# Kernel optimization log

Measured on AMD Instinct MI355X. Metric: run time of the kernel, lower is better.

The kernel has to match this reference:

```python
import jax, jax.numpy as jnp
import numpy as np

T, B, OBS, A, P, NB, H = 32, 256, 1024, 16, 600, 601, 128


def setup_inputs() -> dict:
    key = jax.random.key(0)
    ks = jax.random.split(key, 32)
    f32 = jnp.float32

    def rn(k, shape, scale):
        return jax.random.normal(k, shape, dtype=f32) * scale

    hh = 1.0 / np.sqrt(H)
    inp = {
        "obs_seq": rn(ks[0], (T, B, OBS), 1.0),
        # backbone MLP (512, 512)
        "bb_w1": rn(ks[1], (OBS, 512), 1.0 / np.sqrt(OBS)), "bb_b1": jnp.zeros((512,), f32),
        "bb_w2": rn(ks[2], (512, 512), 1.0 / np.sqrt(512)), "bb_b2": jnp.zeros((512,), f32),
        # feedforward heads (final layers init std=0.01, bias 0 per module)
        "pol_w": rn(ks[3], (512, A), 0.01), "pol_b": jnp.zeros((A,), f32),
        "y_w": rn(ks[4], (512, P), 0.01), "y_b": jnp.zeros((P,), f32),
        "ci_w": rn(ks[5], (512, H), 1.0 / np.sqrt(512)), "ci_b": jnp.zeros((H,), f32),
        # LSTMCell(A, 128): gate order i,f,g,o as in torch
        "w_ih": rn(ks[6], (A, 4 * H), hh), "w_hh": rn(ks[7], (H, 4 * H), hh),
        "b_ih": rn(ks[8], (4 * H,), hh), "b_hh": rn(ks[9], (4 * H,), hh),
        # z / q / aux_pi MLPs: Linear(128,128) -> ReLU -> Linear(128, out)
        "z_w1": rn(ks[10], (H, H), hh), "z_b1": jnp.zeros((H,), f32),
        "z_w2": rn(ks[11], (H, P), 0.01), "z_b2": jnp.zeros((P,), f32),
        "q_w1": rn(ks[12], (H, H), hh), "q_b1": jnp.zeros((H,), f32),
        "q_w2": rn(ks[13], (H, NB), 0.01), "q_b2": jnp.zeros((NB,), f32),
        "a_w1": rn(ks[14], (H, H), hh), "a_b1": jnp.zeros((H,), f32),
        "a_w2": rn(ks[15], (H, A), 0.01), "a_b2": jnp.zeros((A,), f32),
    }
    return inp


def reference(obs_seq, bb_w1, bb_b1, bb_w2, bb_b2, pol_w, pol_b, y_w, y_b,
              ci_w, ci_b, w_ih, w_hh, b_ih, b_hh,
              z_w1, z_b1, z_w2, z_b2, q_w1, q_b1, q_w2, q_b2,
              a_w1, a_b1, a_w2, a_b2):
    Tn, Bn = obs_seq.shape[:2]
    x = obs_seq.reshape(Tn * Bn, -1)  # feedforward across time: fold T into batch
    emb = jax.nn.relu(jax.nn.relu(x @ bb_w1 + bb_b1) @ bb_w2 + bb_b2)  # [N,512]
    logits = emb @ pol_w + pol_b  # [N,A]
    y = emb @ y_w + y_b           # [N,P]
    c0 = emb @ ci_w + ci_b        # [N,H]
    h0 = jnp.tanh(c0)

    # one_hot(a) @ W_ih^T == row a of W_ih (input-to-gate contribution per action)
    in_gates = w_ih + b_ih  # [A, 4H]

    def step(carry, ig):
        h, c = carry
        g = ig + h @ w_hh + b_hh  # [N,4H]
        i, f, gg, o = jnp.split(g, 4, axis=-1)  # torch gate order i,f,g,o
        c = jax.nn.sigmoid(f) * c + jax.nn.sigmoid(i) * jnp.tanh(gg)
        h = jax.nn.sigmoid(o) * jnp.tanh(c)
        return (h, c), h

    _, h_all = jax.lax.scan(step, (h0, c0), in_gates)  # [A, N, H]

    def mlp(hx, w1, b1, w2, b2):
        return jax.nn.relu(hx @ w1 + b1) @ w2 + b2

    def to_tba(arr):
        Aa, N, D = arr.shape
        return arr.reshape(Aa, Tn, Bn, D).transpose(1, 2, 0, 3)  # [T,B,A,D]

    z = to_tba(mlp(h_all, z_w1, z_b1, z_w2, z_b2))
    q = to_tba(mlp(h_all, q_w1, q_b1, q_w2, q_b2))
    aux_pi = to_tba(mlp(h_all, a_w1, a_b1, a_w2, a_b2))
    return (logits.reshape(Tn, Bn, -1), y.reshape(Tn, Bn, -1), z, q, aux_pi)
```

## Files before the change

### kernel.cpp

```cpp
#include <hip/hip_runtime.h>
#include <stdint.h>

typedef short bf16x8 __attribute__((ext_vector_type(8)));
typedef float f32x4 __attribute__((ext_vector_type(4)));
typedef unsigned short u16x4 __attribute__((ext_vector_type(4)));

__device__ __forceinline__ unsigned short f2b(float f) {
  union { float f; unsigned u; } v; v.f = f;
  unsigned r = v.u + 0x7fffu + ((v.u >> 16) & 1u);
  return (unsigned short)(r >> 16);
}
__device__ __forceinline__ float fsigm(float x) { return 1.f / (1.f + __expf(-x)); }
__device__ __forceinline__ float ftanh(float x) {
  float t = __expf(-2.f * fabsf(x));
  float r = (1.f - t) / (1.f + t);
  return copysignf(r, x);
}

struct TD { const float* in; unsigned short* out; int R, C; };
struct TDs { TD d[12]; };

__global__ __launch_bounds__(256) void tconv_all(TDs ds) {
  TD t = ds.d[blockIdx.z];
  int c0 = blockIdx.x * 32, r0 = blockIdx.y * 32;
  if (c0 >= t.C || r0 >= t.R) return;
  __shared__ float tl[32][33];
  int tx = threadIdx.x & 31, ty = threadIdx.x >> 5;
  #pragma unroll
  for (int i = 0; i < 32; i += 8) {
    int r = r0 + ty + i, c = c0 + tx;
    tl[ty + i][tx] = (r < t.R && c < t.C) ? t.in[(size_t)r * t.C + c] : 0.f;
  }
  __syncthreads();
  #pragma unroll
  for (int i = 0; i < 32; i += 8) {
    int c = c0 + ty + i, r = r0 + tx;
    if (c < t.C && r < t.R) t.out[(size_t)c * t.R + r] = f2b(tl[tx][ty + i]);
  }
}

__global__ __launch_bounds__(256) void conv_k(const float* __restrict__ in,
                                              unsigned short* __restrict__ out, int n) {
  int i = (blockIdx.x * 256 + threadIdx.x) * 8;
  if (i >= n) return;
  float4 a = *(const float4*)(in + i);
  float4 b = *(const float4*)(in + i + 4);
  bf16x8 v;
  v[0] = (short)f2b(a.x); v[1] = (short)f2b(a.y); v[2] = (short)f2b(a.z); v[3] = (short)f2b(a.w);
  v[4] = (short)f2b(b.x); v[5] = (short)f2b(b.y); v[6] = (short)f2b(b.z); v[7] = (short)f2b(b.w);
  *(bf16x8*)(out + i) = v;
}

template <int ACT, bool OBF16>
__global__ __launch_bounds__(256) void gemm_k(const unsigned short* __restrict__ A,
                                              const unsigned short* __restrict__ BT,
                                              const float* __restrict__ bias,
                                              void* __restrict__ Cp,
                                              int M, int N, int K, int ldC) {
  __shared__ unsigned short As[64][40];
  __shared__ unsigned short Bs[64][40];
  const int tid = threadIdx.x;
  const int n0 = blockIdx.x * 64;
  const int m0 = blockIdx.y * 64;
  const int wid = tid >> 6, lane = tid & 63;
  const int wm = (wid >> 1) * 32, wn = (wid & 1) * 32;
  const int lr = lane & 15, lk = lane >> 4;
  const int sr = tid >> 2, sc = (tid & 3) * 8;

  f32x4 acc[2][2] = {};

  for (int k0 = 0; k0 < K; k0 += 32) {
    *(bf16x8*)&As[sr][sc] = *(const bf16x8*)(A + (size_t)(m0 + sr) * K + k0 + sc);
    {
      int n = n0 + sr;
      bf16x8 v = {};
      if (n < N) v = *(const bf16x8*)(BT + (size_t)n * K + k0 + sc);
      *(bf16x8*)&Bs[sr][sc] = v;
    }
    __syncthreads();
    bf16x8 af[2], bfr[2];
    #pragma unroll
    for (int mi = 0; mi < 2; mi++) af[mi] = *(const bf16x8*)&As[wm + mi * 16 + lr][lk * 8];
    #pragma unroll
    for (int ni = 0; ni < 2; ni++) bfr[ni] = *(const bf16x8*)&Bs[wn + ni * 16 + lr][lk * 8];
    #pragma unroll
    for (int mi = 0; mi < 2; mi++)
      #pragma unroll
      for (int ni = 0; ni < 2; ni++)
        acc[mi][ni] = __builtin_amdgcn_mfma_f32_16x16x32_bf16(af[mi], bfr[ni], acc[mi][ni], 0, 0, 0);
    __syncthreads();
  }

  #pragma unroll
  for (int mi = 0; mi < 2; mi++)
    #pragma unroll
    for (int ni = 0; ni < 2; ni++) {
      int col = n0 + wn + ni * 16 + lr;
      if (col >= N) continue;
      float bv = bias[col];
      #pragma unroll
      for (int r = 0; r < 4; r++) {
        int row = m0 + wm + mi * 16 + lk * 4 + r;
        float v = acc[mi][ni][r] + bv;
        if (ACT == 1) v = fmaxf(v, 0.f);
        if (OBF16) ((unsigned short*)Cp)[(size_t)row * ldC + col] = f2b(v);
        else       ((float*)Cp)[(size_t)row * ldC + col] = v;
      }
    }
}

__global__ __launch_bounds__(1024) void lstm_k(const float* __restrict__ c0,
                                               const unsigned short* __restrict__ whhT,
                                               const float* __restrict__ w_ih,
                                               const float* __restrict__ b_ih,
                                               const float* __restrict__ b_hh,
                                               unsigned short* __restrict__ h_all) {
  __shared__ float G[32][516];
  __shared__ float cst[32][128];
  __shared__ unsigned short hst[32][136];
  const int tid = threadIdx.x, lane = tid & 63, wid = tid >> 6;
  const int r0 = blockIdx.x * 32;
  const int lr = lane & 15, lk = lane >> 4;

  bf16x8 wv[2][4];
  #pragma unroll
  for (int nj = 0; nj < 2; nj++)
    #pragma unroll
    for (int ks = 0; ks < 4; ks++)
      wv[nj][ks] = *(const bf16x8*)(whhT + (size_t)(wid * 32 + nj * 16 + lr) * 128 + ks * 32 + lk * 8);

  const int j = tid & 127;
  const int rb = tid >> 7;
  const float bs0 = b_ih[j]       + b_hh[j];
  const float bs1 = b_ih[j + 128] + b_hh[j + 128];
  const float bs2 = b_ih[j + 256] + b_hh[j + 256];
  const float bs3 = b_ih[j + 384] + b_hh[j + 384];

  {
    int r = tid >> 5, j4 = (tid & 31) * 4;
    float4 c4 = *(const float4*)(c0 + (size_t)(r0 + r) * 128 + j4);
    *(f32x4*)&cst[r][j4] = f32x4{c4.x, c4.y, c4.z, c4.w};
    u16x4 h4;
    h4[0] = f2b(ftanh(c4.x)); h4[1] = f2b(ftanh(c4.y));
    h4[2] = f2b(ftanh(c4.z)); h4[3] = f2b(ftanh(c4.w));
    *(u16x4*)&hst[r][j4] = h4;
  }
  __syncthreads();

  for (int a = 0; a < 16; a++) {
    f32x4 acc[2][2] = {};
    #pragma unroll
    for (int ks = 0; ks < 4; ks++) {
      bf16x8 af0 = *(const bf16x8*)&hst[lr][ks * 32 + lk * 8];
      bf16x8 af1 = *(const bf16x8*)&hst[16 + lr][ks * 32 + lk * 8];
      #pragma unroll
      for (int nj = 0; nj < 2; nj++) {
        acc[0][nj] = __builtin_amdgcn_mfma_f32_16x16x32_bf16(af0, wv[nj][ks], acc[0][nj], 0, 0, 0);
        acc[1][nj] = __builtin_amdgcn_mfma_f32_16x16x32_bf16(af1, wv[nj][ks], acc[1][nj], 0, 0, 0);
      }
    }
    #pragma unroll
    for (int mi = 0; mi < 2; mi++)
      #pragma unroll
      for (int nj = 0; nj < 2; nj++)
        #pragma unroll
        for (int rr = 0; rr < 4; rr++)
          G[mi * 16 + lk * 4 + rr][wid * 32 + nj * 16 + lr] = acc[mi][nj][rr];
    __syncthreads();

    const float* ig = w_ih + a * 512;
    const float ig0 = ig[j], ig1 = ig[j + 128], ig2 = ig[j + 256], ig3 = ig[j + 384];
    #pragma unroll
    for (int it = 0; it < 4; it++) {
      int r = rb + it * 8;
      float gi = G[r][j]       + ig0 + bs0;
      float gf = G[r][j + 128] + ig1 + bs1;
      float gg = G[r][j + 256] + ig2 + bs2;
      float go = G[r][j + 384] + ig3 + bs3;
      float c = cst[r][j];
      float cn = fsigm(gf) * c + fsigm(gi) * ftanh(gg);
      float h = fsigm(go) * ftanh(cn);
      cst[r][j] = cn;
      unsigned short hb = f2b(h);
      hst[r][j] = hb;
      h_all[((size_t)(r0 + r) * 16 + a) * 128 + j] = hb;
    }
    __syncthreads();
  }
}

__global__ __launch_bounds__(64, 4) void heads_k(
    const unsigned short* __restrict__ hall,
    const unsigned short* __restrict__ w1cat,
    const unsigned short* __restrict__ w2cat,
    const float* __restrict__ zb1, const float* __restrict__ qb1, const float* __restrict__ ab1,
    const float* __restrict__ zb2, const float* __restrict__ qb2, const float* __restrict__ ab2,
    float* __restrict__ oz, float* __restrict__ oq, float* __restrict__ oa) {
  __shared__ unsigned short hp[32][136];
  const int lane = threadIdx.x & 63;
  const int lr = lane & 15, lk = lane >> 4;
  const int r0 = blockIdx.x * 32;

  const float* B1a[3] = {zb1, qb1, ab1};
  const float* B2a[3] = {zb2, qb2, ab2};
  float*       OOa[3] = {oz, oq, oa};

  #pragma unroll
  for (int hi = 0; hi < 3; hi++) {
    const int Nh    = (hi == 0) ? 600 : (hi == 1) ? 601 : 16;
    const int so    = (hi == 0) ? 0 : (hi == 1) ? 600 : 1201;
    const int NFULL = Nh >> 4;
    const int TAIL  = Nh & 15;
    const float* b1 = B1a[hi];
    const float* b2 = B2a[hi];
    float* Oh = OOa[hi];

    {
      bf16x8 av[2][4];
      #pragma unroll
      for (int jf = 0; jf < 2; jf++)
        #pragma unroll
        for (int ks = 0; ks < 4; ks++)
          av[jf][ks] = *(const bf16x8*)(hall + (size_t)(r0 + jf * 16 + lr) * 128 + ks * 32 + lk * 8);
      #pragma unroll
      for (int nf = 0; nf < 8; nf++) {
        bf16x8 w1v[4];
        #pragma unroll
        for (int ks = 0; ks < 4; ks++)
          w1v[ks] = *(const bf16x8*)(w1cat + (size_t)(hi * 128 + nf * 16 + lr) * 128 + ks * 32 + lk * 8);
        f32x4 hacc[2] = {};
        #pragma unroll
        for (int ks = 0; ks < 4; ks++)
          #pragma unroll
          for (int jf = 0; jf < 2; jf++)
            hacc[jf] = __builtin_amdgcn_mfma_f32_16x16x32_bf16(w1v[ks], av[jf][ks], hacc[jf], 0, 0, 0);
        f32x4 bb = *(const f32x4*)(b1 + nf * 16 + lk * 4);
        #pragma unroll
        for (int jf = 0; jf < 2; jf++) {
          u16x4 h4;
          #pragma unroll
          for (int rr = 0; rr < 4; rr++)
            h4[rr] = f2b(fmaxf(hacc[jf][rr] + bb[rr], 0.f));
          *(u16x4*)&hp[jf * 16 + lr][nf * 16 + lk * 4] = h4;
        }
      }
    }
    asm volatile("s_waitcnt lgkmcnt(0)" ::: "memory");
    __builtin_amdgcn_sched_barrier(0);

    bf16x8 hv[2][4];
    #pragma unroll
    for (int jf = 0; jf < 2; jf++)
      #pragma unroll
      for (int ks = 0; ks < 4; ks++)
        hv[jf][ks] = *(const bf16x8*)&hp[jf * 16 + lr][ks * 32 + lk * 8];

    bf16x8 wA[4], wB[4];
    {
      int rowb = min(lr, Nh - 1);
      #pragma unroll
      for (int ks = 0; ks < 4; ks++)
        wA[ks] = *(const bf16x8*)(w2cat + (size_t)(so + rowb) * 128 + ks * 32 + lk * 8);
    }
    const int NFT = NFULL + (TAIL ? 1 : 0);
    for (int fo = 0; fo < NFULL; fo++) {
      int fn = fo + 1;
      if (fn < NFT) {
        int rowb = min(fn * 16 + lr, Nh - 1);
        #pragma unroll
        for (int ks = 0; ks < 4; ks++)
          wB[ks] = *(const bf16x8*)(w2cat + (size_t)(so + rowb) * 128 + ks * 32 + lk * 8);
      }
      f32x4 oacc[2] = {};
      #pragma unroll
      for (int ks = 0; ks < 4; ks++)
        #pragma unroll
        for (int jf = 0; jf < 2; jf++)
          oacc[jf] = __builtin_amdgcn_mfma_f32_16x16x32_bf16(wA[ks], hv[jf][ks], oacc[jf], 0, 0, 0);
      f32x4 bb = *(const f32x4*)(b2 + fo * 16 + lk * 4);
      #pragma unroll
      for (int jf = 0; jf < 2; jf++) {
        f32x4 v = oacc[jf] + bb;
        float* p = Oh + (size_t)(r0 + jf * 16 + lr) * Nh + fo * 16 + lk * 4;
        __builtin_memcpy(p, &v, 16);
      }
      #pragma unroll
      for (int ks = 0; ks < 4; ks++) wA[ks] = wB[ks];
    }
    if (TAIL) {
      f32x4 oacc[2] = {};
      #pragma unroll
      for (int ks = 0; ks < 4; ks++)
        #pragma unroll
        for (int jf = 0; jf < 2; jf++)
          oacc[jf] = __builtin_amdgcn_mfma_f32_16x16x32_bf16(wA[ks], hv[jf][ks], oacc[jf], 0, 0, 0);
      #pragma unroll
      for (int jf = 0; jf < 2; jf++)
        #pragma unroll
        for (int rr = 0; rr < 4; rr++) {
          int col = NFULL * 16 + lk * 4 + rr;
          if (col < Nh)
            Oh[(size_t)(r0 + jf * 16 + lr) * Nh + col] = oacc[jf][rr] + b2[col];
        }
    }
  }
}

extern "C" void kernel_launch(void* const* d_in, const int* in_sizes, int n_in,
                              void* d_out, int out_size, void* d_ws, size_t ws_size,
                              hipStream_t stream) {
  const float* obs   = (const float*)d_in[0];
  const float* bb_w1 = (const float*)d_in[1];
  const float* bb_b1 = (const float*)d_in[2];
  const float* bb_w2 = (const float*)d_in[3];
  const float* bb_b2 = (const float*)d_in[4];
  const float* pol_w = (const float*)d_in[5];
  const float* pol_b = (const float*)d_in[6];
  const float* y_w   = (const float*)d_in[7];
  const float* y_b   = (const float*)d_in[8];
  const float* ci_w  = (const float*)d_in[9];
  const float* ci_b  = (const float*)d_in[10];
  const float* w_ih  = (const float*)d_in[11];
  const float* w_hh  = (const float*)d_in[12];
  const float* b_ih  = (const float*)d_in[13];
  const float* b_hh  = (const float*)d_in[14];
  const float* z_w1  = (const float*)d_in[15];
  const float* z_b1  = (const float*)d_in[16];
  const float* z_w2  = (const float*)d_in[17];
  const float* z_b2  = (const float*)d_in[18];
  const float* q_w1  = (const float*)d_in[19];
  const float* q_b1  = (const float*)d_in[20];
  const float* q_w2  = (const float*)d_in[21];
  const float* q_b2  = (const float*)d_in[22];
  const float* a_w1  = (const float*)d_in[23];
  const float* a_b1  = (const float*)d_in[24];
  const float* a_w2  = (const float*)d_in[25];
  const float* a_b2  = (const float*)d_in[26];

  float* out = (float*)d_out;
  float* out_logits = out;
  float* out_y      = out + 131072;
  float* out_z      = out + 5046272;
  float* out_q      = out + 83689472;
  float* out_a      = out + 162463744;

  uint8_t* ws = (uint8_t*)d_ws;
  size_t off = 0;
  auto alc = [&](size_t bytes) -> void* {
    void* p = ws + off;
    off = (off + bytes + 255) & ~(size_t)255;
    return p;
  };
  unsigned short* W1T  = (unsigned short*)alc((size_t)512 * 1024 * 2);
  unsigned short* W2T  = (unsigned short*)alc((size_t)512 * 512 * 2);
  unsigned short* polT = (unsigned short*)alc((size_t)16 * 512 * 2);
  unsigned short* yT   = (unsigned short*)alc((size_t)600 * 512 * 2);
  unsigned short* ciT  = (unsigned short*)alc((size_t)128 * 512 * 2);
  unsigned short* whhT = (unsigned short*)alc((size_t)512 * 128 * 2);
  unsigned short* zw1T = (unsigned short*)alc((size_t)128 * 128 * 2);
  unsigned short* qw1T = (unsigned short*)alc((size_t)128 * 128 * 2);
  unsigned short* aw1T = (unsigned short*)alc((size_t)128 * 128 * 2);
  unsigned short* zw2T = (unsigned short*)alc((size_t)600 * 128 * 2);
  unsigned short* qw2T = (unsigned short*)alc((size_t)601 * 128 * 2);
  unsigned short* aw2T = (unsigned short*)alc((size_t)16 * 128 * 2);
  unsigned short* obsb = (unsigned short*)alc((size_t)8192 * 1024 * 2);
  unsigned short* hid1 = (unsigned short*)alc((size_t)8192 * 512 * 2);
  unsigned short* emb  = (unsigned short*)alc((size_t)8192 * 512 * 2);
  float*          c0b  = (float*)alc((size_t)8192 * 128 * 4);
  unsigned short* hall = (unsigned short*)alc((size_t)8192 * 16 * 128 * 2);
  (void)ws_size; (void)in_sizes; (void)n_in; (void)out_size;

  dim3 B256(256);

  TDs td;
  td.d[0]  = {bb_w1, W1T, 1024, 512};
  td.d[1]  = {bb_w2, W2T, 512, 512};
  td.d[2]  = {pol_w, polT, 512, 16};
  td.d[3]  = {y_w,   yT,   512, 600};
  td.d[4]  = {ci_w,  ciT,  512, 128};
  td.d[5]  = {w_hh,  whhT, 128, 512};
  td.d[6]  = {z_w1,  zw1T, 128, 128};
  td.d[7]  = {z_w2,  zw2T, 128, 600};
  td.d[8]  = {q_w1,  qw1T, 128, 128};
  td.d[9]  = {q_w2,  qw2T, 128, 601};
  td.d[10] = {a_w1,  aw1T, 128, 128};
  td.d[11] = {a_w2,  aw2T, 128, 16};
  tconv_all<<<dim3(19, 32, 12), B256, 0, stream>>>(td);

  conv_k<<<dim3(4096), B256, 0, stream>>>(obs, obsb, 8192 * 1024);

  gemm_k<1, true><<<dim3(8, 128), B256, 0, stream>>>(obsb, W1T, bb_b1, hid1, 8192, 512, 1024, 512);
  gemm_k<1, true><<<dim3(8, 128), B256, 0, stream>>>(hid1, W2T, bb_b2, emb,  8192, 512, 512,  512);
  gemm_k<0, false><<<dim3(1, 128),  B256, 0, stream>>>(emb, polT, pol_b, out_logits, 8192, 16,  512, 16);
  gemm_k<0, false><<<dim3(10, 128), B256, 0, stream>>>(emb, yT,   y_b,   out_y,      8192, 600, 512, 600);
  gemm_k<0, false><<<dim3(2, 128),  B256, 0, stream>>>(emb, ciT,  ci_b,  c0b,        8192, 128, 512, 128);
  lstm_k<<<dim3(256), dim3(1024), 0, stream>>>(c0b, whhT, w_ih, b_ih, b_hh, hall);
  heads_k<<<dim3(4096), dim3(64), 0, stream>>>(hall,
                                               zw1T, zw2T,
                                               z_b1, q_b1, a_b1,
                                               z_b2, q_b2, a_b2,
                                               out_z, out_q, out_a);
}
```

Baseline: 506.7 us.

## Split head MLPs into hidden-layer kernel and LDS-tiled output GEMM kernels

Replaces the single per-wave heads kernel with a hidden-layer kernel that writes z and q ReLU activations to global memory (finishing the small aux head in place), plus templated output kernels. These stage a 208-column slice of the second-layer weights in swizzled shared memory and reuse it across 256 rows per block. Previously each 64-thread block re-read all of w2 from global or L2 for only 32 rows. The split adds a round trip of the bf16 hidden activations (about 64 MB written and read) and reuses the obs staging buffer as scratch.

```diff
diff --git a/kernel.cpp b/kernel.cpp
--- a/kernel.cpp
+++ b/kernel.cpp
@@ -189,119 +189,156 @@
   }
 }
 
-__global__ __launch_bounds__(64, 4) void heads_k(
+__global__ __launch_bounds__(256, 4) void hidden_k(
     const unsigned short* __restrict__ hall,
     const unsigned short* __restrict__ w1cat,
-    const unsigned short* __restrict__ w2cat,
+    const unsigned short* __restrict__ w2a,
     const float* __restrict__ zb1, const float* __restrict__ qb1, const float* __restrict__ ab1,
-    const float* __restrict__ zb2, const float* __restrict__ qb2, const float* __restrict__ ab2,
-    float* __restrict__ oz, float* __restrict__ oq, float* __restrict__ oa) {
-  __shared__ unsigned short hp[32][136];
-  const int lane = threadIdx.x & 63;
+    const float* __restrict__ ab2,
+    unsigned short* __restrict__ hhz, unsigned short* __restrict__ hhq,
+    float* __restrict__ oa) {
+  __shared__ float bls[384];
+  __shared__ unsigned short hp[4][32][136];
+  const int tid = threadIdx.x, lane = tid & 63, wid = tid >> 6;
   const int lr = lane & 15, lk = lane >> 4;
-  const int r0 = blockIdx.x * 32;
-
-  const float* B1a[3] = {zb1, qb1, ab1};
-  const float* B2a[3] = {zb2, qb2, ab2};
-  float*       OOa[3] = {oz, oq, oa};
+  const int r0 = blockIdx.x * 128 + wid * 32;
+
+  if (tid < 128) { bls[tid] = zb1[tid]; bls[256 + tid] = ab1[tid]; }
+  else if (tid < 256) bls[tid] = qb1[tid - 128];
+  __syncthreads();
+
+  bf16x8 av[2][4];
+  #pragma unroll
+  for (int jf = 0; jf < 2; jf++)
+    #pragma unroll
+    for (int ks = 0; ks < 4; ks++)
+      av[jf][ks] = *(const bf16x8*)(hall + (size_t)(r0 + jf * 16 + lr) * 128 + ks * 32 + lk * 8);
 
   #pragma unroll
   for (int hi = 0; hi < 3; hi++) {
-    const int Nh    = (hi == 0) ? 600 : (hi == 1) ? 601 : 16;
-    const int so    = (hi == 0) ? 0 : (hi == 1) ? 600 : 1201;
-    const int NFULL = Nh >> 4;
-    const int TAIL  = Nh & 15;
-    const float* b1 = B1a[hi];
-    const float* b2 = B2a[hi];
-    float* Oh = OOa[hi];
-
-    {
-      bf16x8 av[2][4];
-      #pragma unroll
-      for (int jf = 0; jf < 2; jf++)
-        #pragma unroll
-        for (int ks = 0; ks < 4; ks++)
-          av[jf][ks] = *(const bf16x8*)(hall + (size_t)(r0 + jf * 16 + lr) * 128 + ks * 32 + lk * 8);
-      #pragma unroll
-      for (int nf = 0; nf < 8; nf++) {
-        bf16x8 w1v[4];
-        #pragma unroll
-        for (int ks = 0; ks < 4; ks++)
-          w1v[ks] = *(const bf16x8*)(w1cat + (size_t)(hi * 128 + nf * 16 + lr) * 128 + ks * 32 + lk * 8);
-        f32x4 hacc[2] = {};
-        #pragma unroll
-        for (int ks = 0; ks < 4; ks++)
-          #pragma unroll
-          for (int jf = 0; jf < 2; jf++)
-            hacc[jf] = __builtin_amdgcn_mfma_f32_16x16x32_bf16(w1v[ks], av[jf][ks], hacc[jf], 0, 0, 0);
-        f32x4 bb = *(const f32x4*)(b1 + nf * 16 + lk * 4);
-        #pragma unroll
-        for (int jf = 0; jf < 2; jf++) {
-          u16x4 h4;
-          #pragma unroll
-          for (int rr = 0; rr < 4; rr++)
-            h4[rr] = f2b(fmaxf(hacc[jf][rr] + bb[rr], 0.f));
-          *(u16x4*)&hp[jf * 16 + lr][nf * 16 + lk * 4] = h4;
-        }
-      }
-    }
-    asm volatile("s_waitcnt lgkmcnt(0)" ::: "memory");
-    __builtin_amdgcn_sched_barrier(0);
-
-    bf16x8 hv[2][4];
-    #pragma unroll
-    for (int jf = 0; jf < 2; jf++)
+    unsigned short* hh = (hi == 0) ? hhz : hhq;
+    #pragma unroll
+    for (int nf = 0; nf < 8; nf++) {
+      bf16x8 w1v[4];
       #pragma unroll
       for (int ks = 0; ks < 4; ks++)
-        hv[jf][ks] = *(const bf16x8*)&hp[jf * 16 + lr][ks * 32 + lk * 8];
-
-    bf16x8 wA[4], wB[4];
-    {
-      int rowb = min(lr, Nh - 1);
-      #pragma unroll
-      for (int ks = 0; ks < 4; ks++)
-        wA[ks] = *(const bf16x8*)(w2cat + (size_t)(so + rowb) * 128 + ks * 32 + lk * 8);
-    }
-    const int NFT = NFULL + (TAIL ? 1 : 0);
-    for (int fo = 0; fo < NFULL; fo++) {
-      int fn = fo + 1;
-      if (fn < NFT) {
-        int rowb = min(fn * 16 + lr, Nh - 1);
-        #pragma unroll
-        for (int ks = 0; ks < 4; ks++)
-          wB[ks] = *(const bf16x8*)(w2cat + (size_t)(so + rowb) * 128 + ks * 32 + lk * 8);
-      }
-      f32x4 oacc[2] = {};
+        w1v[ks] = *(const bf16x8*)(w1cat + (size_t)(hi * 128 + nf * 16 + lr) * 128 + ks * 32 + lk * 8);
+      f32x4 hacc[2] = {};
       #pragma unroll
       for (int ks = 0; ks < 4; ks++)
         #pragma unroll
         for (int jf = 0; jf < 2; jf++)
-          oacc[jf] = __builtin_amdgcn_mfma_f32_16x16x32_bf16(wA[ks], hv[jf][ks], oacc[jf], 0, 0, 0);
-      f32x4 bb = *(const f32x4*)(b2 + fo * 16 + lk * 4);
+          hacc[jf] = __builtin_amdgcn_mfma_f32_16x16x32_bf16(w1v[ks], av[jf][ks], hacc[jf], 0, 0, 0);
+      f32x4 bb = *(const f32x4*)&bls[hi * 128 + nf * 16 + lk * 4];
       #pragma unroll
       for (int jf = 0; jf < 2; jf++) {
-        f32x4 v = oacc[jf] + bb;
-        float* p = Oh + (size_t)(r0 + jf * 16 + lr) * Nh + fo * 16 + lk * 4;
-        __builtin_memcpy(p, &v, 16);
+        u16x4 h4;
+        #pragma unroll
+        for (int rr = 0; rr < 4; rr++)
+          h4[rr] = f2b(fmaxf(hacc[jf][rr] + bb[rr], 0.f));
+        if (hi < 2)
+          *(u16x4*)(hh + (size_t)(r0 + jf * 16 + lr) * 128 + nf * 16 + lk * 4) = h4;
+        else
+          *(u16x4*)&hp[wid][jf * 16 + lr][nf * 16 + lk * 4] = h4;
       }
-      #pragma unroll
-      for (int ks = 0; ks < 4; ks++) wA[ks] = wB[ks];
-    }
-    if (TAIL) {
-      f32x4 oacc[2] = {};
-      #pragma unroll
-      for (int ks = 0; ks < 4; ks++)
+    }
+  }
+
+  asm volatile("s_waitcnt lgkmcnt(0)" ::: "memory");
+  __builtin_amdgcn_sched_barrier(0);
+
+  bf16x8 hv[2][4];
+  #pragma unroll
+  for (int jf = 0; jf < 2; jf++)
+    #pragma unroll
+    for (int ks = 0; ks < 4; ks++)
+      hv[jf][ks] = *(const bf16x8*)&hp[wid][jf * 16 + lr][ks * 32 + lk * 8];
+  bf16x8 wa[4];
+  #pragma unroll
+  for (int ks = 0; ks < 4; ks++)
+    wa[ks] = *(const bf16x8*)(w2a + (size_t)lr * 128 + ks * 32 + lk * 8);
+  f32x4 oacc[2] = {};
+  #pragma unroll
+  for (int ks = 0; ks < 4; ks++)
+    #pragma unroll
+    for (int jf = 0; jf < 2; jf++)
+      oacc[jf] = __builtin_amdgcn_mfma_f32_16x16x32_bf16(wa[ks], hv[jf][ks], oacc[jf], 0, 0, 0);
+  f32x4 bbo = *(const f32x4*)(ab2 + lk * 4);
+  #pragma unroll
+  for (int jf = 0; jf < 2; jf++) {
+    f32x4 v = oacc[jf] + bbo;
+    *(f32x4*)(oa + (size_t)(r0 + jf * 16 + lr) * 16 + lk * 4) = v;
+  }
+}
+
+template <int NH>
+__global__ __launch_bounds__(256, 2) void out_k(
+    const unsigned short* __restrict__ hh,
+    const unsigned short* __restrict__ w2,
+    const float* __restrict__ b2,
+    float* __restrict__ O) {
+  __shared__ unsigned short wls[208 * 128];
+  __shared__ float bls[208];
+  const int tid = threadIdx.x, lane = tid & 63, wid = tid >> 6;
+  const int lr = lane & 15, lk = lane >> 4;
+  const int r0 = blockIdx.x * 256 + wid * 64;
+  const int gf0 = blockIdx.y * 13;
+
+  #pragma unroll
+  for (int it = 0; it < 13; it++) {
+    int row = it * 16 + (tid >> 4);
+    int slot = tid & 15;
+    int gr = gf0 * 16 + row; if (gr > NH - 1) gr = NH - 1;
+    bf16x8 v = *(const bf16x8*)(w2 + (size_t)gr * 128 + ((slot ^ (row & 7)) << 3));
+    *(bf16x8*)&wls[row * 128 + slot * 8] = v;
+  }
+  if (tid < 52) {
+    int col = gf0 * 16 + tid * 4;
+    f32x4 b = {};
+    #pragma unroll
+    for (int r = 0; r < 4; r++) b[r] = (col + r < NH) ? b2[col + r] : 0.f;
+    *(f32x4*)&bls[tid * 4] = b;
+  }
+
+  bf16x8 av[4][4];
+  #pragma unroll
+  for (int mi = 0; mi < 4; mi++)
+    #pragma unroll
+    for (int ks = 0; ks < 4; ks++)
+      av[mi][ks] = *(const bf16x8*)(hh + (size_t)(r0 + mi * 16 + lr) * 128 + ks * 32 + lk * 8);
+  __syncthreads();
+
+  for (int f = 0; f < 13; f++) {
+    int wrow = f * 16 + lr;
+    bf16x8 wv[4];
+    #pragma unroll
+    for (int ks = 0; ks < 4; ks++) {
+      int sl = (ks * 4 + lk) ^ (wrow & 7);
+      wv[ks] = *(const bf16x8*)&wls[wrow * 128 + sl * 8];
+    }
+    f32x4 oacc[4] = {};
+    #pragma unroll
+    for (int ks = 0; ks < 4; ks++)
+      #pragma unroll
+      for (int mi = 0; mi < 4; mi++)
+        oacc[mi] = __builtin_amdgcn_mfma_f32_16x16x32_bf16(wv[ks], av[mi][ks], oacc[mi], 0, 0, 0);
+    f32x4 bb = *(const f32x4*)&bls[f * 16 + lk * 4];
+    int col = (gf0 + f) * 16 + lk * 4;
+    if (col + 3 < NH) {
+      #pragma unroll
+      for (int mi = 0; mi < 4; mi++) {
+        f32x4 v = oacc[mi] + bb;
+        float* p = O + (size_t)(r0 + mi * 16 + lr) * NH + col;
+        if (NH % 4 == 0) *(f32x4*)p = v;
+        else __builtin_memcpy(p, &v, 16);
+      }
+    } else if (col < NH) {
+      #pragma unroll
+      for (int mi = 0; mi < 4; mi++)
         #pragma unroll
-        for (int jf = 0; jf < 2; jf++)
-          oacc[jf] = __builtin_amdgcn_mfma_f32_16x16x32_bf16(wA[ks], hv[jf][ks], oacc[jf], 0, 0, 0);
-      #pragma unroll
-      for (int jf = 0; jf < 2; jf++)
-        #pragma unroll
-        for (int rr = 0; rr < 4; rr++) {
-          int col = NFULL * 16 + lk * 4 + rr;
-          if (col < Nh)
-            Oh[(size_t)(r0 + jf * 16 + lr) * Nh + col] = oacc[jf][rr] + b2[col];
-        }
+        for (int rr = 0; rr < 4; rr++)
+          if (col + rr < NH)
+            O[(size_t)(r0 + mi * 16 + lr) * NH + col + rr] = oacc[mi][rr] + bb[rr];
     }
   }
 }
@@ -368,6 +405,8 @@
   unsigned short* emb  = (unsigned short*)alc((size_t)8192 * 512 * 2);
   float*          c0b  = (float*)alc((size_t)8192 * 128 * 4);
   unsigned short* hall = (unsigned short*)alc((size_t)8192 * 16 * 128 * 2);
+  unsigned short* hhz  = obsb;
+  unsigned short* hhq  = (unsigned short*)alc((size_t)131072 * 128 * 2);
   (void)ws_size; (void)in_sizes; (void)n_in; (void)out_size;
 
   dim3 B256(256);
@@ -395,9 +434,9 @@
   gemm_k<0, false><<<dim3(10, 128), B256, 0, stream>>>(emb, yT,   y_b,   out_y,      8192, 600, 512, 600);
   gemm_k<0, false><<<dim3(2, 128),  B256, 0, stream>>>(emb, ciT,  ci_b,  c0b,        8192, 128, 512, 128);
   lstm_k<<<dim3(256), dim3(1024), 0, stream>>>(c0b, whhT, w_ih, b_ih, b_hh, hall);
-  heads_k<<<dim3(4096), dim3(64), 0, stream>>>(hall,
-                                               zw1T, zw2T,
-                                               z_b1, q_b1, a_b1,
-                                               z_b2, q_b2, a_b2,
-                                               out_z, out_q, out_a);
-}
+  hidden_k<<<dim3(1024), B256, 0, stream>>>(hall, zw1T, aw2T,
+                                            z_b1, q_b1, a_b1, a_b2,
+                                            hhz, hhq, out_a);
+  out_k<600><<<dim3(512, 3), B256, 0, stream>>>(hhz, zw2T, z_b2, out_z);
+  out_k<601><<<dim3(512, 3), B256, 0, stream>>>(hhq, qw2T, q_b2, out_q);
+}
```

After: 488.7 us. 1.04x faster.
